# Kernel tuning notes

Hardware: AMD Instinct MI355X
Metric: run time of the kernel (lower is better)

Reference implementation:

```python
import jax, jax.numpy as jnp
import numpy as np

T1, T2 = 10.0, 50.0          # Canny hysteresis thresholds from EdgeNorm
HYST_ITERS = 16              # fixed-iteration approximation of Canny hysteresis BFS
TEMPERATURE = 1.0
NUM_CLASSES_M1 = 13.0


def _shift(a, dy, dx):
    # zero-padded shift of [n,h,w]
    p = jnp.pad(a, ((0, 0), (1, 1), (1, 1)))
    return jax.lax.dynamic_slice(p, (0, 1 + dy, 1 + dx), a.shape)


def _sobel(img):
    # img: [n,h,w] float32; replicate border, aperture-3 Sobel (cv2.Canny default)
    p = jnp.pad(img, ((0, 0), (1, 1), (1, 1)), mode='edge')[:, None]  # [n,1,h+2,w+2]
    kx = jnp.array([[-1, 0, 1], [-2, 0, 2], [-1, 0, 1]], jnp.float32)
    ky = jnp.array([[-1, -2, -1], [0, 0, 0], [1, 2, 1]], jnp.float32)
    k = jnp.stack([kx, ky])[:, None]                                  # [2,1,3,3]
    g = jax.lax.conv_general_dilated(p, k, (1, 1), 'VALID')           # [n,2,h,w]
    return g[:, 0], g[:, 1]


def _canny(img_u8):
    # vectorized Canny over the batch (cv2 loops per sample on CPU)
    img = img_u8.astype(jnp.float32)
    gx, gy = _sobel(img)
    mag = jnp.abs(gx) + jnp.abs(gy)                 # L1 magnitude (cv2 L2gradient=False)
    ang = jnp.mod(jnp.degrees(jnp.arctan2(gy, gx)), 180.0)
    s0 = (ang < 22.5) | (ang >= 157.5)
    s45 = (ang >= 22.5) & (ang < 67.5)
    s90 = (ang >= 67.5) & (ang < 112.5)
    # non-max suppression: compare along quantized gradient direction
    n1 = jnp.where(s0, _shift(mag, 0, 1),
         jnp.where(s45, _shift(mag, -1, 1),
         jnp.where(s90, _shift(mag, -1, 0), _shift(mag, -1, -1))))
    n2 = jnp.where(s0, _shift(mag, 0, -1),
         jnp.where(s45, _shift(mag, 1, -1),
         jnp.where(s90, _shift(mag, 1, 0), _shift(mag, 1, 1))))
    nms = jnp.where((mag >= n1) & (mag >= n2), mag, 0.0)
    strong = nms > T2
    weak = nms > T1

    def body(_, s):
        grown = jax.lax.reduce_window(s.astype(jnp.float32), -jnp.inf, jax.lax.max,
                                      (1, 3, 3), (1, 1, 1),
                                      [(0, 0), (1, 1), (1, 1)]) > 0.0
        return grown & weak

    strong = jax.lax.fori_loop(0, HYST_ITERS, body, strong)
    return strong.astype(jnp.float32) * 255.0       # [n,h,w] in {0,255}


def _dilate_blur(edges):
    # cv2.dilate with 10x10 ones kernel, anchor=(5,5) -> asymmetric (5,4) window pad
    d = jax.lax.reduce_window(edges, -jnp.inf, jax.lax.max,
                              (1, 10, 10), (1, 1, 1),
                              [(0, 0), (5, 4), (5, 4)])
    # cv2.blur 10x10 box filter, reflect101 border, rounded back to uint8
    p = jnp.pad(d, ((0, 0), (5, 4), (5, 4)), mode='reflect')
    b = jax.lax.reduce_window(p, 0.0, jax.lax.add,
                              (1, 10, 10), (1, 1, 1), 'VALID') / 100.0
    return jnp.round(b) / 255.0                     # EdgeNorm: e / 255


def setup_inputs() -> dict:
    key = jax.random.key(0)
    k1, k2 = jax.random.split(key)
    n, c, h, w = 8, 14, 512, 512
    return {
        'preds_S': jax.random.normal(k1, (n, c, h, w), dtype=jnp.float32),
        'preds_T': jax.random.normal(k2, (n, c, h, w), dtype=jnp.float32),
    }


def reference(preds_S, preds_T):
    n, c, h, w = preds_S.shape
    # teacher argmax map -> uint8 grayscale (truncating cast, as torch .type(uint8))
    t_map = (jnp.argmax(preds_T, axis=1).astype(jnp.float32)
             / NUM_CLASSES_M1 * 255.0).astype(jnp.uint8)
    edges = jax.lax.stop_gradient(_dilate_blur(_canny(t_map)))  # [n,h,w], constant wrt grads
    pred_T = edges[:, None] * preds_T
    pred_S = edges[:, None] * preds_S
    # ChannelNorm: softmax over flattened h*w per (n,c); divergence='kl' -> norm_s.log()
    logsm_t = jax.nn.log_softmax(pred_T.reshape(n, c, h * w), axis=-1)
    logsm_s = jax.nn.log_softmax(pred_S.reshape(n, c, h * w), axis=-1)
    norm_t = jnp.exp(logsm_t)
    loss = jnp.sum(norm_t * (logsm_t - logsm_s))    # KLDivLoss(reduction='sum')
    loss = loss / (n * c)                           # channel norm divisor
    return loss * (TEMPERATURE ** 2)
```

## Files before the change

### kernel.cpp

```cpp
#include <hip/hip_runtime.h>
#include <math.h>

#define NB 8
#define CC 14
#define HH 512
#define WW 512
#define HW (HH*WW)
#define NHW (NB*HW)
#define WPR 8
#define WPI (HH*WPR)
#define KSPLIT 16
#define KCHUNK (HW/KSPLIT)

typedef unsigned long long u64;

__global__ __launch_bounds__(256) void k_argmax(const float* __restrict__ T,
                                                unsigned char* __restrict__ tmap) {
    int i = blockIdx.x * blockDim.x + threadIdx.x;
    if (i >= NHW) return;
    int n = i / HW;
    int p = i - n * HW;
    const float* base = T + (size_t)n * CC * HW + p;
    float best = base[0];
    int bi = 0;
#pragma unroll
    for (int c = 1; c < CC; ++c) {
        float v = base[(size_t)c * HW];
        if (v > best) { best = v; bi = c; }
    }
    float g = ((float)bi / 13.0f) * 255.0f;
    tmap[i] = (unsigned char)g;
}

__global__ __launch_bounds__(256) void k_sobel(const unsigned char* __restrict__ tmap,
                                               unsigned short* __restrict__ m16) {
    int i = blockIdx.x * blockDim.x + threadIdx.x;
    if (i >= NHW) return;
    int n = i / HW;
    int p = i - n * HW;
    int y = p / WW;
    int x = p - y * WW;
    const unsigned char* im = tmap + (size_t)n * HW;
    int ym = y > 0 ? y - 1 : 0, yp = y < HH - 1 ? y + 1 : HH - 1;
    int xm = x > 0 ? x - 1 : 0, xp = x < WW - 1 ? x + 1 : WW - 1;
    int a00 = im[ym * WW + xm], a01 = im[ym * WW + x], a02 = im[ym * WW + xp];
    int a10 = im[y  * WW + xm],                        a12 = im[y  * WW + xp];
    int a20 = im[yp * WW + xm], a21 = im[yp * WW + x], a22 = im[yp * WW + xp];
    int gx = (a02 - a00) + 2 * (a12 - a10) + (a22 - a20);
    int gy = (a20 - a00) + 2 * (a21 - a01) + (a22 - a02);
    int m = (gx < 0 ? -gx : gx) + (gy < 0 ? -gy : gy);
    float ang = atan2f((float)gy, (float)gx) * 57.29577951308232f;
    ang = fmodf(ang, 180.0f);
    if (ang < 0.0f) ang += 180.0f;
    int s;
    if (ang < 22.5f || ang >= 157.5f) s = 0;
    else if (ang < 67.5f)             s = 1;
    else if (ang < 112.5f)            s = 2;
    else                              s = 3;
    m16[i] = (unsigned short)((m << 2) | s);
}

__global__ __launch_bounds__(256) void k_nms(const unsigned short* __restrict__ m16,
                                             u64* __restrict__ weakBits,
                                             u64* __restrict__ strongBits) {
    int i = blockIdx.x * blockDim.x + threadIdx.x;
    int n = i / HW;
    int p = i - n * HW;
    int y = p / WW;
    int x = p - y * WW;
    const unsigned short* mp = m16 + (size_t)n * HW;
    int v = mp[p];
    int mc = v >> 2;
    int s = v & 3;
    int dy1, dx1, dy2, dx2;
    if (s == 0)      { dy1 = 0;  dx1 = 1;  dy2 = 0; dx2 = -1; }
    else if (s == 1) { dy1 = -1; dx1 = 1;  dy2 = 1; dx2 = -1; }
    else if (s == 2) { dy1 = -1; dx1 = 0;  dy2 = 1; dx2 = 0;  }
    else             { dy1 = -1; dx1 = -1; dy2 = 1; dx2 = 1;  }
    int y1 = y + dy1, x1 = x + dx1, y2 = y + dy2, x2 = x + dx2;
    int n1 = (y1 < 0 || y1 >= HH || x1 < 0 || x1 >= WW) ? 0 : (mp[y1 * WW + x1] >> 2);
    int n2 = (y2 < 0 || y2 >= HH || x2 < 0 || x2 >= WW) ? 0 : (mp[y2 * WW + x2] >> 2);
    int nms = (mc >= n1 && mc >= n2) ? mc : 0;
    u64 wm = __ballot(nms > 10);
    u64 sm = __ballot(nms > 50);
    if ((threadIdx.x & 63) == 0) {
        weakBits[i >> 6]   = wm;
        strongBits[i >> 6] = sm;
    }
}

#define HALO 21
#define TROWS (256 + 2*HALO)
__global__ __launch_bounds__(1024) void k_hyst_dil(const u64* __restrict__ strongBits,
                                                   const u64* __restrict__ weakBits,
                                                   u64* __restrict__ dilBits) {
    int blk  = blockIdx.x;
    int n    = blk >> 1;
    int half = blk & 1;
    int g0   = half * 256 - HALO;
    __shared__ u64 A[TROWS * WPR];
    __shared__ u64 B[TROWS * WPR];
    __shared__ u64 Wl[TROWS * WPR];
    int tid = threadIdx.x;

    for (int idx = tid; idx < TROWS * WPR; idx += 1024) {
        int vr = g0 + (idx >> 3);
        int w  = idx & 7;
        u64 sv = 0, wv = 0;
        if (vr >= 0 && vr < HH) {
            sv = strongBits[(size_t)n * WPI + vr * WPR + w];
            wv = weakBits  [(size_t)n * WPI + vr * WPR + w];
        }
        A[idx] = sv;
        Wl[idx] = wv;
    }
    __syncthreads();

    for (int it = 0; it < 16; ++it) {
        const u64* src = (it & 1) ? B : A;
        u64*       dst = (it & 1) ? A : B;
        for (int idx = tid; idx < TROWS * WPR; idx += 1024) {
            int r = idx >> 3;
            int w = idx & 7;
            u64 c  = src[idx];
            u64 up = (r > 0)         ? src[idx - 8] : 0;
            u64 dn = (r < TROWS - 1) ? src[idx + 8] : 0;
            u64 a = c | up | dn;
            u64 pL = 0, pR = 0;
            if (w > 0) {
                u64 cl = src[idx - 1];
                u64 ul = (r > 0)         ? src[idx - 9] : 0;
                u64 dl = (r < TROWS - 1) ? src[idx + 7] : 0;
                pL = cl | ul | dl;
            }
            if (w < 7) {
                u64 cr = src[idx + 1];
                u64 ur = (r > 0)         ? src[idx - 7] : 0;
                u64 dr = (r < TROWS - 1) ? src[idx + 9] : 0;
                pR = cr | ur | dr;
            }
            u64 g = a | (a << 1) | (pL >> 63) | (a >> 1) | (pR << 63);
            dst[idx] = g & Wl[idx];
        }
        __syncthreads();
    }

    for (int idx = tid; idx < TROWS * WPR; idx += 1024) {
        int w = idx & 7;
        u64 v  = A[idx];
        u64 p  = (w > 0) ? A[idx - 1] : 0;
        u64 nx = (w < 7) ? A[idx + 1] : 0;
        u64 o = v;
#pragma unroll
        for (int d = 1; d <= 5; ++d) o |= (v << d) | (p >> (64 - d));
#pragma unroll
        for (int d = 1; d <= 4; ++d) o |= (v >> d) | (nx << (64 - d));
        B[idx] = o;
    }
    __syncthreads();

    for (int idx = tid; idx < 256 * WPR; idx += 1024) {
        int rr = idx >> 3;
        int w  = idx & 7;
        int r  = rr + HALO;
        u64 o = 0;
#pragma unroll
        for (int dy = -5; dy <= 4; ++dy) o |= B[(r + dy) * WPR + w];
        int outrow = half * 256 + rr;
        dilBits[(size_t)n * WPI + outrow * WPR + w] = o;
    }
}

__global__ __launch_bounds__(256) void k_blur(const u64* __restrict__ dilBits,
                                              float* __restrict__ E) {
    int n  = blockIdx.y;
    int y0 = blockIdx.x * 64;
    __shared__ u64 rows[74 * WPR];
    __shared__ unsigned char rc[74 * 512];
    int tid = threadIdx.x;

    for (int idx = tid; idx < 74 * WPR; idx += 256) {
        int vi = idx >> 3;
        int w  = idx & 7;
        int v  = y0 - 5 + vi;
        int r  = v < 0 ? -v : (v > HH - 1 ? 2 * (HH - 1) - v : v);
        rows[idx] = dilBits[(size_t)n * WPI + r * WPR + w];
    }
    __syncthreads();

    for (int idx = tid; idx < 74 * 512; idx += 256) {
        int r = idx >> 9;
        int x = idx & 511;
        int c;
        if (x >= 5 && x <= 507) {
            int b = x - 5, wd = b >> 6, off = b & 63;
            u64 v = rows[r * WPR + wd] >> off;
            if (off && wd < 7) v |= rows[r * WPR + wd + 1] << (64 - off);
            c = __popcll(v & 0x3FFull);
        } else {
            c = 0;
            for (int dx = -5; dx <= 4; ++dx) {
                int xx = x + dx;
                xx = xx < 0 ? -xx : (xx > WW - 1 ? 2 * (WW - 1) - xx : xx);
                c += (int)((rows[r * WPR + (xx >> 6)] >> (xx & 63)) & 1ull);
            }
        }
        rc[idx] = (unsigned char)c;
    }
    __syncthreads();

    for (int idx = tid; idx < 64 * 512; idx += 256) {
        int yy = idx >> 9;
        int x  = idx & 511;
        int sum = 0;
#pragma unroll
        for (int k = 0; k < 10; ++k) sum += rc[(yy + k) * 512 + x];
        float b = rintf((255.0f * (float)sum) / 100.0f);
        E[(size_t)n * HW + (y0 + yy) * WW + x] = b / 255.0f;
    }
}

__global__ __launch_bounds__(256) void k_kl_partial(const float* __restrict__ S,
                                                    const float* __restrict__ T,
                                                    const float* __restrict__ E,
                                                    double* __restrict__ partial) {
    int cidx  = blockIdx.x;
    int split = blockIdx.y;
    int n = cidx / CC;
    const float4* Tp = (const float4*)(T + (size_t)cidx * HW + (size_t)split * KCHUNK);
    const float4* Sp = (const float4*)(S + (size_t)cidx * HW + (size_t)split * KCHUNK);
    const float4* Ep = (const float4*)(E + (size_t)n    * HW + (size_t)split * KCHUNK);
    int tid = threadIdx.x;

    float Zt = 0.0f, Wt = 0.0f, Zs = 0.0f;
#pragma unroll
    for (int k = 0; k < KCHUNK / 4 / 256; ++k) {
        int j = k * 256 + tid;
        float4 t4 = Tp[j];
        float4 s4 = Sp[j];
        float4 e4 = Ep[j];
#pragma unroll
        for (int u = 0; u < 4; ++u) {
            float e = (&e4.x)[u];
            float t = e * (&t4.x)[u];
            float s = e * (&s4.x)[u];
            float et = __expf(t);
            Zt += et;
            Wt += et * (t - s);
            Zs += __expf(s);
        }
    }

    __shared__ double r1[256], r2[256], r3[256];
    r1[tid] = (double)Zt; r2[tid] = (double)Wt; r3[tid] = (double)Zs;
    __syncthreads();
    for (int off = 128; off > 0; off >>= 1) {
        if (tid < off) {
            r1[tid] += r1[tid + off];
            r2[tid] += r2[tid + off];
            r3[tid] += r3[tid + off];
        }
        __syncthreads();
    }
    if (tid == 0) {
        double* o = partial + ((size_t)cidx * KSPLIT + split) * 3;
        o[0] = r1[0]; o[1] = r2[0]; o[2] = r3[0];
    }
}

__global__ __launch_bounds__(128) void k_kl_final(const double* __restrict__ partial,
                                                  float* __restrict__ out) {
    int tid = threadIdx.x;
    double loss = 0.0;
    if (tid < NB * CC) {
        double Zt = 0.0, Wt = 0.0, Zs = 0.0;
        for (int sp = 0; sp < KSPLIT; ++sp) {
            const double* p = partial + ((size_t)tid * KSPLIT + sp) * 3;
            Zt += p[0]; Wt += p[1]; Zs += p[2];
        }
        loss = Wt / Zt - log(Zt) + log(Zs);
    }
    __shared__ double red[128];
    red[tid] = loss;
    __syncthreads();
    for (int off = 64; off > 0; off >>= 1) {
        if (tid < off) red[tid] += red[tid + off];
        __syncthreads();
    }
    if (tid == 0) out[0] = (float)(red[0] / (double)(NB * CC));
}

extern "C" void kernel_launch(void* const* d_in, const int* in_sizes, int n_in,
                              void* d_out, int out_size, void* d_ws, size_t ws_size,
                              hipStream_t stream) {
    const float* S = (const float*)d_in[0];
    const float* T = (const float*)d_in[1];
    float* out = (float*)d_out;

    char* ws = (char*)d_ws;
    float*          e_buf      = (float*)(ws);
    unsigned short* m16        = (unsigned short*)(ws + (size_t)NHW * 4);
    unsigned char*  tmap       = (unsigned char*)(ws + (size_t)NHW * 6);
    u64*            weakBits   = (u64*)(ws + (size_t)NHW * 7);
    u64*            strongBits = (u64*)(ws + (size_t)NHW * 7 + (NHW/8));
    u64*            dilBits    = (u64*)(ws + (size_t)NHW * 7 + 2*(NHW/8));
    double*         partial    = (double*)(ws + (size_t)NHW * 7 + 3*(NHW/8));

    dim3 blk(256);
    dim3 grd(NHW / 256);

    k_argmax<<<grd, blk, 0, stream>>>(T, tmap);
    k_sobel <<<grd, blk, 0, stream>>>(tmap, m16);
    k_nms   <<<grd, blk, 0, stream>>>(m16, weakBits, strongBits);
    k_hyst_dil<<<dim3(NB * 2), dim3(1024), 0, stream>>>(strongBits, weakBits, dilBits);
    k_blur  <<<dim3(8, NB), blk, 0, stream>>>(dilBits, e_buf);
    k_kl_partial<<<dim3(NB * CC, KSPLIT), blk, 0, stream>>>(S, T, e_buf, partial);
    k_kl_final<<<1, 128, 0, stream>>>(partial, out);
    (void)in_sizes; (void)n_in; (void)out_size; (void)ws_size;
}
```

Baseline: 352.3 us.

## Fuse Sobel with NMS, retile hysteresis, vectorize argmax, slide blur window

The argmax now reads float4 and writes four teacher-map bytes per thread. Sobel and non-max suppression are fused into one shared-memory tiled kernel, which removes the 16-bit magnitude buffer round trip. Hysteresis and dilation now run on 64-row tiles with a 21-row halo across 64 blocks instead of 16, which raises parallelism at the cost of redundant halo work. The blur now uses a running vertical sum over 32-row tiles, and the KL split factor is doubled. Together these aim to cut memory traffic and launch overhead and to fix the underfilled hysteresis stage. The split change relies on the unseen final reduction indexing the extra partials correctly.

```diff
diff --git a/kernel.cpp b/kernel.cpp
--- a/kernel.cpp
+++ b/kernel.cpp
@@ -9,177 +9,195 @@
 #define NHW (NB*HW)
 #define WPR 8
 #define WPI (HH*WPR)
-#define KSPLIT 16
+#define KSPLIT 32
 #define KCHUNK (HW/KSPLIT)
 
 typedef unsigned long long u64;
 
 __global__ __launch_bounds__(256) void k_argmax(const float* __restrict__ T,
-                                                unsigned char* __restrict__ tmap) {
-    int i = blockIdx.x * blockDim.x + threadIdx.x;
-    if (i >= NHW) return;
-    int n = i / HW;
-    int p = i - n * HW;
-    const float* base = T + (size_t)n * CC * HW + p;
-    float best = base[0];
-    int bi = 0;
+                                                uchar4* __restrict__ tmap4) {
+    int i4 = blockIdx.x * blockDim.x + threadIdx.x;
+    if (i4 >= NHW / 4) return;
+    int n  = i4 / (HW / 4);
+    int p4 = i4 - n * (HW / 4);
+    const float4* base = (const float4*)(T + (size_t)n * CC * HW) + p4;
+    float4 best = base[0];
+    int b0 = 0, b1 = 0, b2 = 0, b3 = 0;
 #pragma unroll
     for (int c = 1; c < CC; ++c) {
-        float v = base[(size_t)c * HW];
-        if (v > best) { best = v; bi = c; }
-    }
-    float g = ((float)bi / 13.0f) * 255.0f;
-    tmap[i] = (unsigned char)g;
-}
-
-__global__ __launch_bounds__(256) void k_sobel(const unsigned char* __restrict__ tmap,
-                                               unsigned short* __restrict__ m16) {
-    int i = blockIdx.x * blockDim.x + threadIdx.x;
-    if (i >= NHW) return;
-    int n = i / HW;
-    int p = i - n * HW;
-    int y = p / WW;
-    int x = p - y * WW;
+        float4 v = base[(size_t)c * (HW / 4)];
+        if (v.x > best.x) { best.x = v.x; b0 = c; }
+        if (v.y > best.y) { best.y = v.y; b1 = c; }
+        if (v.z > best.z) { best.z = v.z; b2 = c; }
+        if (v.w > best.w) { best.w = v.w; b3 = c; }
+    }
+    uchar4 g;
+    g.x = (unsigned char)(((float)b0 / 13.0f) * 255.0f);
+    g.y = (unsigned char)(((float)b1 / 13.0f) * 255.0f);
+    g.z = (unsigned char)(((float)b2 / 13.0f) * 255.0f);
+    g.w = (unsigned char)(((float)b3 / 13.0f) * 255.0f);
+    tmap4[i4] = g;
+}
+
+__global__ __launch_bounds__(256) void k_sobel_nms(const unsigned char* __restrict__ tmap,
+                                                   u64* __restrict__ weakBits,
+                                                   u64* __restrict__ strongBits) {
+    int tx = blockIdx.x, ty = blockIdx.y, n = blockIdx.z;
+    int x0 = tx * 64, y0 = ty * 64;
+    __shared__ unsigned char tm[68 * 68];
+    __shared__ unsigned short ms[66 * 66];
+    int tid = threadIdx.x;
     const unsigned char* im = tmap + (size_t)n * HW;
-    int ym = y > 0 ? y - 1 : 0, yp = y < HH - 1 ? y + 1 : HH - 1;
-    int xm = x > 0 ? x - 1 : 0, xp = x < WW - 1 ? x + 1 : WW - 1;
-    int a00 = im[ym * WW + xm], a01 = im[ym * WW + x], a02 = im[ym * WW + xp];
-    int a10 = im[y  * WW + xm],                        a12 = im[y  * WW + xp];
-    int a20 = im[yp * WW + xm], a21 = im[yp * WW + x], a22 = im[yp * WW + xp];
-    int gx = (a02 - a00) + 2 * (a12 - a10) + (a22 - a20);
-    int gy = (a20 - a00) + 2 * (a21 - a01) + (a22 - a02);
-    int m = (gx < 0 ? -gx : gx) + (gy < 0 ? -gy : gy);
-    float ang = atan2f((float)gy, (float)gx) * 57.29577951308232f;
-    ang = fmodf(ang, 180.0f);
-    if (ang < 0.0f) ang += 180.0f;
-    int s;
-    if (ang < 22.5f || ang >= 157.5f) s = 0;
-    else if (ang < 67.5f)             s = 1;
-    else if (ang < 112.5f)            s = 2;
-    else                              s = 3;
-    m16[i] = (unsigned short)((m << 2) | s);
-}
-
-__global__ __launch_bounds__(256) void k_nms(const unsigned short* __restrict__ m16,
-                                             u64* __restrict__ weakBits,
-                                             u64* __restrict__ strongBits) {
-    int i = blockIdx.x * blockDim.x + threadIdx.x;
-    int n = i / HW;
-    int p = i - n * HW;
-    int y = p / WW;
-    int x = p - y * WW;
-    const unsigned short* mp = m16 + (size_t)n * HW;
-    int v = mp[p];
-    int mc = v >> 2;
-    int s = v & 3;
-    int dy1, dx1, dy2, dx2;
-    if (s == 0)      { dy1 = 0;  dx1 = 1;  dy2 = 0; dx2 = -1; }
-    else if (s == 1) { dy1 = -1; dx1 = 1;  dy2 = 1; dx2 = -1; }
-    else if (s == 2) { dy1 = -1; dx1 = 0;  dy2 = 1; dx2 = 0;  }
-    else             { dy1 = -1; dx1 = -1; dy2 = 1; dx2 = 1;  }
-    int y1 = y + dy1, x1 = x + dx1, y2 = y + dy2, x2 = x + dx2;
-    int n1 = (y1 < 0 || y1 >= HH || x1 < 0 || x1 >= WW) ? 0 : (mp[y1 * WW + x1] >> 2);
-    int n2 = (y2 < 0 || y2 >= HH || x2 < 0 || x2 >= WW) ? 0 : (mp[y2 * WW + x2] >> 2);
-    int nms = (mc >= n1 && mc >= n2) ? mc : 0;
-    u64 wm = __ballot(nms > 10);
-    u64 sm = __ballot(nms > 50);
-    if ((threadIdx.x & 63) == 0) {
-        weakBits[i >> 6]   = wm;
-        strongBits[i >> 6] = sm;
+
+    for (int idx = tid; idx < 68 * 68; idx += 256) {
+        int r = idx / 68, c = idx - r * 68;
+        int yy = y0 - 2 + r; yy = yy < 0 ? 0 : (yy > HH - 1 ? HH - 1 : yy);
+        int xx = x0 - 2 + c; xx = xx < 0 ? 0 : (xx > WW - 1 ? WW - 1 : xx);
+        tm[idx] = im[yy * WW + xx];
+    }
+    __syncthreads();
+
+    for (int idx = tid; idx < 66 * 66; idx += 256) {
+        int r = idx / 66, c = idx - r * 66;
+        const unsigned char* t0 = tm + r * 68 + c;
+        int a00 = t0[0],   a01 = t0[1],   a02 = t0[2];
+        int a10 = t0[68],                 a12 = t0[70];
+        int a20 = t0[136], a21 = t0[137], a22 = t0[138];
+        int gx = (a02 - a00) + 2 * (a12 - a10) + (a22 - a20);
+        int gy = (a20 - a00) + 2 * (a21 - a01) + (a22 - a02);
+        int m = (gx < 0 ? -gx : gx) + (gy < 0 ? -gy : gy);
+        float ang = atan2f((float)gy, (float)gx) * 57.29577951308232f;
+        ang = fmodf(ang, 180.0f);
+        if (ang < 0.0f) ang += 180.0f;
+        int s;
+        if (ang < 22.5f || ang >= 157.5f) s = 0;
+        else if (ang < 67.5f)             s = 1;
+        else if (ang < 112.5f)            s = 2;
+        else                              s = 3;
+        ms[idx] = (unsigned short)((m << 2) | s);
+    }
+    __syncthreads();
+
+    int lane = tid & 63;
+    int warp = tid >> 6;
+#pragma unroll
+    for (int it = 0; it < 16; ++it) {
+        int row = it * 4 + warp;
+        int gy_ = y0 + row, gx_ = x0 + lane;
+        int v = ms[(row + 1) * 66 + (lane + 1)];
+        int mc = v >> 2, s = v & 3;
+        int dy1, dx1, dy2, dx2;
+        if (s == 0)      { dy1 = 0;  dx1 = 1;  dy2 = 0; dx2 = -1; }
+        else if (s == 1) { dy1 = -1; dx1 = 1;  dy2 = 1; dx2 = -1; }
+        else if (s == 2) { dy1 = -1; dx1 = 0;  dy2 = 1; dx2 = 0;  }
+        else             { dy1 = -1; dx1 = -1; dy2 = 1; dx2 = 1;  }
+        int y1 = gy_ + dy1, x1 = gx_ + dx1, y2 = gy_ + dy2, x2 = gx_ + dx2;
+        int n1 = (y1 < 0 || y1 >= HH || x1 < 0 || x1 >= WW)
+                 ? 0 : (ms[(row + 1 + dy1) * 66 + (lane + 1 + dx1)] >> 2);
+        int n2 = (y2 < 0 || y2 >= HH || x2 < 0 || x2 >= WW)
+                 ? 0 : (ms[(row + 1 + dy2) * 66 + (lane + 1 + dx2)] >> 2);
+        int nms = (mc >= n1 && mc >= n2) ? mc : 0;
+        u64 wm = __ballot(nms > 10);
+        u64 sm = __ballot(nms > 50);
+        if (lane == 0) {
+            size_t w = (size_t)n * WPI + gy_ * WPR + tx;
+            weakBits[w]   = wm;
+            strongBits[w] = sm;
+        }
     }
 }
 
 #define HALO 21
-#define TROWS (256 + 2*HALO)
+#define TROWS (64 + 2*HALO)
+#define TWORDS (TROWS * WPR)
 __global__ __launch_bounds__(1024) void k_hyst_dil(const u64* __restrict__ strongBits,
                                                    const u64* __restrict__ weakBits,
                                                    u64* __restrict__ dilBits) {
-    int blk  = blockIdx.x;
-    int n    = blk >> 1;
-    int half = blk & 1;
-    int g0   = half * 256 - HALO;
-    __shared__ u64 A[TROWS * WPR];
-    __shared__ u64 B[TROWS * WPR];
-    __shared__ u64 Wl[TROWS * WPR];
-    int tid = threadIdx.x;
-
-    for (int idx = tid; idx < TROWS * WPR; idx += 1024) {
-        int vr = g0 + (idx >> 3);
-        int w  = idx & 7;
+    int tile = blockIdx.x & 7;
+    int n    = blockIdx.x >> 3;
+    int g0   = tile * 64 - HALO;
+    __shared__ u64 A[TWORDS];
+    __shared__ u64 B[TWORDS];
+    __shared__ u64 Wl[TWORDS];
+    int tid = threadIdx.x;
+
+    if (tid < TWORDS) {
+        int vr = g0 + (tid >> 3);
+        int w  = tid & 7;
         u64 sv = 0, wv = 0;
         if (vr >= 0 && vr < HH) {
             sv = strongBits[(size_t)n * WPI + vr * WPR + w];
             wv = weakBits  [(size_t)n * WPI + vr * WPR + w];
         }
-        A[idx] = sv;
-        Wl[idx] = wv;
-    }
-    __syncthreads();
-
+        A[tid] = sv;
+        Wl[tid] = wv;
+    }
+    __syncthreads();
+
+#pragma unroll 1
     for (int it = 0; it < 16; ++it) {
         const u64* src = (it & 1) ? B : A;
         u64*       dst = (it & 1) ? A : B;
-        for (int idx = tid; idx < TROWS * WPR; idx += 1024) {
-            int r = idx >> 3;
-            int w = idx & 7;
-            u64 c  = src[idx];
-            u64 up = (r > 0)         ? src[idx - 8] : 0;
-            u64 dn = (r < TROWS - 1) ? src[idx + 8] : 0;
+        if (tid < TWORDS) {
+            int r = tid >> 3;
+            int w = tid & 7;
+            u64 c  = src[tid];
+            u64 up = (r > 0)         ? src[tid - 8] : 0;
+            u64 dn = (r < TROWS - 1) ? src[tid + 8] : 0;
             u64 a = c | up | dn;
             u64 pL = 0, pR = 0;
             if (w > 0) {
-                u64 cl = src[idx - 1];
-                u64 ul = (r > 0)         ? src[idx - 9] : 0;
-                u64 dl = (r < TROWS - 1) ? src[idx + 7] : 0;
+                u64 cl = src[tid - 1];
+                u64 ul = (r > 0)         ? src[tid - 9] : 0;
+                u64 dl = (r < TROWS - 1) ? src[tid + 7] : 0;
                 pL = cl | ul | dl;
             }
             if (w < 7) {
-                u64 cr = src[idx + 1];
-                u64 ur = (r > 0)         ? src[idx - 7] : 0;
-                u64 dr = (r < TROWS - 1) ? src[idx + 9] : 0;
+                u64 cr = src[tid + 1];
+                u64 ur = (r > 0)         ? src[tid - 7] : 0;
+                u64 dr = (r < TROWS - 1) ? src[tid + 9] : 0;
                 pR = cr | ur | dr;
             }
             u64 g = a | (a << 1) | (pL >> 63) | (a >> 1) | (pR << 63);
-            dst[idx] = g & Wl[idx];
+            dst[tid] = g & Wl[tid];
         }
         __syncthreads();
     }
 
-    for (int idx = tid; idx < TROWS * WPR; idx += 1024) {
-        int w = idx & 7;
-        u64 v  = A[idx];
-        u64 p  = (w > 0) ? A[idx - 1] : 0;
-        u64 nx = (w < 7) ? A[idx + 1] : 0;
+    if (tid < TWORDS) {
+        int w = tid & 7;
+        u64 v  = A[tid];
+        u64 p  = (w > 0) ? A[tid - 1] : 0;
+        u64 nx = (w < 7) ? A[tid + 1] : 0;
         u64 o = v;
 #pragma unroll
         for (int d = 1; d <= 5; ++d) o |= (v << d) | (p >> (64 - d));
 #pragma unroll
         for (int d = 1; d <= 4; ++d) o |= (v >> d) | (nx << (64 - d));
-        B[idx] = o;
-    }
-    __syncthreads();
-
-    for (int idx = tid; idx < 256 * WPR; idx += 1024) {
-        int rr = idx >> 3;
-        int w  = idx & 7;
+        B[tid] = o;
+    }
+    __syncthreads();
+
+    if (tid < 64 * WPR) {
+        int rr = tid >> 3;
+        int w  = tid & 7;
         int r  = rr + HALO;
         u64 o = 0;
 #pragma unroll
         for (int dy = -5; dy <= 4; ++dy) o |= B[(r + dy) * WPR + w];
-        int outrow = half * 256 + rr;
-        dilBits[(size_t)n * WPI + outrow * WPR + w] = o;
+        dilBits[(size_t)n * WPI + (tile * 64 + rr) * WPR + w] = o;
     }
 }
 
 __global__ __launch_bounds__(256) void k_blur(const u64* __restrict__ dilBits,
                                               float* __restrict__ E) {
     int n  = blockIdx.y;
-    int y0 = blockIdx.x * 64;
-    __shared__ u64 rows[74 * WPR];
-    __shared__ unsigned char rc[74 * 512];
-    int tid = threadIdx.x;
-
-    for (int idx = tid; idx < 74 * WPR; idx += 256) {
+    int y0 = blockIdx.x * 32;
+    __shared__ u64 rows[42 * WPR];
+    __shared__ unsigned char rc[42 * 512];
+    int tid = threadIdx.x;
+
+    for (int idx = tid; idx < 42 * WPR; idx += 256) {
         int vi = idx >> 3;
         int w  = idx & 7;
         int v  = y0 - 5 + vi;
@@ -188,7 +206,7 @@
     }
     __syncthreads();
 
-    for (int idx = tid; idx < 74 * 512; idx += 256) {
+    for (int idx = tid; idx < 42 * 512; idx += 256) {
         int r = idx >> 9;
         int x = idx & 511;
         int c;
@@ -209,14 +227,16 @@
     }
     __syncthreads();
 
-    for (int idx = tid; idx < 64 * 512; idx += 256) {
-        int yy = idx >> 9;
-        int x  = idx & 511;
+    for (int x = tid; x < 512; x += 256) {
         int sum = 0;
 #pragma unroll
-        for (int k = 0; k < 10; ++k) sum += rc[(yy + k) * 512 + x];
-        float b = rintf((255.0f * (float)sum) / 100.0f);
-        E[(size_t)n * HW + (y0 + yy) * WW + x] = b / 255.0f;
+        for (int k = 0; k < 10; ++k) sum += rc[k * 512 + x];
+        float* o = E + (size_t)n * HW + y0 * WW + x;
+        o[0] = rintf((255.0f * (float)sum) / 100.0f) / 255.0f;
+        for (int yy = 1; yy < 32; ++yy) {
+            sum += (int)rc[(yy + 9) * 512 + x] - (int)rc[(yy - 1) * 512 + x];
+            o[yy * WW] = rintf((255.0f * (float)sum) / 100.0f) / 255.0f;
+        }
     }
 }
 
@@ -298,23 +318,18 @@
     float* out = (float*)d_out;
 
     char* ws = (char*)d_ws;
-    float*          e_buf      = (float*)(ws);
-    unsigned short* m16        = (unsigned short*)(ws + (size_t)NHW * 4);
-    unsigned char*  tmap       = (unsigned char*)(ws + (size_t)NHW * 6);
-    u64*            weakBits   = (u64*)(ws + (size_t)NHW * 7);
-    u64*            strongBits = (u64*)(ws + (size_t)NHW * 7 + (NHW/8));
-    u64*            dilBits    = (u64*)(ws + (size_t)NHW * 7 + 2*(NHW/8));
-    double*         partial    = (double*)(ws + (size_t)NHW * 7 + 3*(NHW/8));
-
-    dim3 blk(256);
-    dim3 grd(NHW / 256);
-
-    k_argmax<<<grd, blk, 0, stream>>>(T, tmap);
-    k_sobel <<<grd, blk, 0, stream>>>(tmap, m16);
-    k_nms   <<<grd, blk, 0, stream>>>(m16, weakBits, strongBits);
-    k_hyst_dil<<<dim3(NB * 2), dim3(1024), 0, stream>>>(strongBits, weakBits, dilBits);
-    k_blur  <<<dim3(8, NB), blk, 0, stream>>>(dilBits, e_buf);
-    k_kl_partial<<<dim3(NB * CC, KSPLIT), blk, 0, stream>>>(S, T, e_buf, partial);
+    float*         e_buf      = (float*)(ws);
+    unsigned char* tmap       = (unsigned char*)(ws + (size_t)NHW * 4);
+    u64*           weakBits   = (u64*)(ws + (size_t)NHW * 5);
+    u64*           strongBits = (u64*)(ws + (size_t)NHW * 5 + (NHW/8));
+    u64*           dilBits    = (u64*)(ws + (size_t)NHW * 5 + 2*(NHW/8));
+    double*        partial    = (double*)(ws + (size_t)NHW * 5 + 3*(NHW/8));
+
+    k_argmax<<<dim3(NHW / 4 / 256), dim3(256), 0, stream>>>(T, (uchar4*)tmap);
+    k_sobel_nms<<<dim3(8, 8, NB), dim3(256), 0, stream>>>(tmap, weakBits, strongBits);
+    k_hyst_dil<<<dim3(NB * 8), dim3(1024), 0, stream>>>(strongBits, weakBits, dilBits);
+    k_blur<<<dim3(16, NB), dim3(256), 0, stream>>>(dilBits, e_buf);
+    k_kl_partial<<<dim3(NB * CC, KSPLIT), dim3(256), 0, stream>>>(S, T, e_buf, partial);
     k_kl_final<<<1, 128, 0, stream>>>(partial, out);
     (void)in_sizes; (void)n_in; (void)out_size; (void)ws_size;
 }
```

Result: faster. 315.3 us (-10.5%).
